# Kernel optimization log

Measured on AMD Instinct MI355X. Metric: run time of the kernel, lower is better.

Reference implementation:

```python
import jax, jax.numpy as jnp
import numpy as np

TEMPERATURE = 0.5
EPS = 1e-8  # torch cosine_similarity norm clamp


def setup_inputs() -> dict:
    key = jax.random.key(0)
    k1, k2, k3 = jax.random.split(key, 3)
    N, D = 4096, 256
    z_i = jax.random.normal(k1, (N, D), dtype=jnp.float32)
    z_j = jax.random.normal(k2, (N, D), dtype=jnp.float32)
    weights = jax.random.uniform(k3, (N,), dtype=jnp.float32)
    return {"z_i": z_i, "z_j": z_j, "weights": weights}


def reference(z_i, z_j, weights):
    N = z_i.shape[0]
    z = jnp.concatenate([z_i, z_j], axis=0)  # [2N, D]
    # cosine similarity via normalized matmul (same math as broadcasted F.cosine_similarity)
    norm = jnp.maximum(jnp.linalg.norm(z, axis=1, keepdims=True), EPS)
    zn = z / norm
    sim = zn @ zn.T  # [2N, 2N]
    # positives: diagonals at offsets +N and -N
    sim_ij = jnp.diagonal(sim, offset=N)
    sim_ji = jnp.diagonal(sim, offset=-N)
    positives = jnp.concatenate([sim_ij, sim_ji], axis=0)  # [2N]
    mask = 1.0 - jnp.eye(2 * N, dtype=sim.dtype)
    denominator = jnp.sum(mask * jnp.exp(sim / TEMPERATURE), axis=1)  # [2N]
    numerator = jnp.exp(positives / TEMPERATURE)
    all_losses = -jnp.log(numerator / denominator)  # [2N]
    w2 = jnp.tile(weights, 2)  # weights.repeat(2)
    loss = jnp.sum(all_losses * w2) / jnp.sum(w2)
    return loss
```

## Files before the change

### kernel.cpp

```cpp
#include <hip/hip_runtime.h>
#include <hip/hip_bf16.h>

#define PN   4096
#define PN2  8192
#define PD   256
#define TILE 128
#define NBLK (PN2 / TILE)
#define NTRI (NBLK * (NBLK + 1) / 2)

typedef __attribute__((ext_vector_type(8))) short bf16x8;
typedef __attribute__((ext_vector_type(4))) float f32x4;

typedef const __attribute__((address_space(1))) void* gas_ptr;
typedef __attribute__((address_space(3))) void* las_ptr;


__global__ __launch_bounds__(256) void normalize_kernel(
    const float* __restrict__ zi, const float* __restrict__ zj,
    __hip_bfloat16* __restrict__ zn, float* __restrict__ rowsum) {
  int r = blockIdx.x;
  int tid = threadIdx.x;
  const float* src = (r < PN) ? (zi + (size_t)r * PD) : (zj + (size_t)(r - PN) * PD);
  float x = src[tid];
  float s = x * x;
  #pragma unroll
  for (int off = 32; off >= 1; off >>= 1) s += __shfl_xor(s, off, 64);
  __shared__ float p[4];
  if ((tid & 63) == 0) p[tid >> 6] = s;
  __syncthreads();
  float tot = p[0] + p[1] + p[2] + p[3];
  float nrm = fmaxf(sqrtf(tot), 1e-8f);
  int g  = r >> 4, rr = r & 15;
  int c  = tid >> 5, q = (tid >> 3) & 3, j = tid & 7;
  zn[(size_t)(g * 8 + c) * 512 + q * 128 + rr * 8 + j] = __float2bfloat16(x / nrm);
  if (tid == 0) rowsum[r] = 0.0f;
}

__global__ __launch_bounds__(256, 2) void simsum_kernel(
    const __hip_bfloat16* __restrict__ zn,
    float* __restrict__ rowsum, float* __restrict__ pos) {
  __shared__ char As[64 * 1024];

  const int idx = blockIdx.x;
  int bj = (int)((sqrtf(8.0f * (float)idx + 1.0f) - 1.0f) * 0.5f);
  while ((bj + 1) * (bj + 2) / 2 <= idx) ++bj;
  while (bj * (bj + 1) / 2 > idx) --bj;
  const int bi = idx - bj * (bj + 1) / 2;
  const bool diagBlk = (bi == bj);
  const bool posBlk  = (bj == bi + PN / TILE);

  const int tid  = threadIdx.x;
  const int wave = tid >> 6;
  const int lane = tid & 63;
  const int quad = lane >> 4;
  const int c16  = lane & 15;
  const int wrow = bi * TILE + (wave >> 1) * 64;
  const int wcol = bj * TILE + (wave & 1) * 64;

  const char* aslab = (const char*)zn + (size_t)bi * 65536;
  #pragma unroll
  for (int p = 0; p < 16; ++p) {
    int off = (p * 4 + wave) * 1024;
    __builtin_amdgcn_global_load_lds((gas_ptr)(aslab + off + lane * 16),
                                     (las_ptr)(As + off), 16, 0, 0);
  }

  const __hip_bfloat16* bB[4];
  #pragma unroll
  for (int i = 0; i < 4; ++i)
    bB[i] = zn + (size_t)(bj * 8 + (wave & 1) * 4 + i) * 4096 + lane * 8;

  f32x4 acc[4][4];
  #pragma unroll
  for (int i = 0; i < 4; ++i)
    #pragma unroll
    for (int j = 0; j < 4; ++j)
      acc[i][j] = (f32x4){0.f, 0.f, 0.f, 0.f};

  const int arowg = (wave >> 1) * 4;

  __syncthreads();

  #pragma unroll
  for (int c = 0; c < 8; ++c) {
    bf16x8 a[4], b[4];
    #pragma unroll
    for (int ni = 0; ni < 4; ++ni) b[ni] = *(const bf16x8*)(bB[ni] + c * 512);
    #pragma unroll
    for (int mi = 0; mi < 4; ++mi)
      a[mi] = *(const bf16x8*)(As + ((arowg + mi) * 8 + c) * 1024 + lane * 16);
    #pragma unroll
    for (int mi = 0; mi < 4; ++mi)
      #pragma unroll
      for (int ni = 0; ni < 4; ++ni)
        acc[mi][ni] = __builtin_amdgcn_mfma_f32_16x16x32_bf16(a[mi], b[ni], acc[mi][ni], 0, 0, 0);
  }

  float colsum[4] = {0.f, 0.f, 0.f, 0.f};
  #pragma unroll
  for (int mi = 0; mi < 4; ++mi) {
    int rbase = wrow + mi * 16 + quad * 4;
    float rs[4] = {0.f, 0.f, 0.f, 0.f};
    #pragma unroll
    for (int ni = 0; ni < 4; ++ni) {
      int gcol = wcol + ni * 16 + c16;
      #pragma unroll
      for (int t = 0; t < 4; ++t) {
        int grow = rbase + t;
        float sim = acc[mi][ni][t];
        float e = __expf(2.0f * sim);
        if (diagBlk && gcol == grow) e = 0.0f;
        rs[t] += e;
        colsum[ni] += e;
        if (posBlk && gcol == grow + PN) {
          pos[grow] = sim;
          pos[grow + PN] = sim;
        }
      }
    }
    #pragma unroll
    for (int t = 0; t < 4; ++t) {
      #pragma unroll
      for (int off = 1; off <= 8; off <<= 1) rs[t] += __shfl_xor(rs[t], off, 64);
    }
    if (c16 == 0) {
      #pragma unroll
      for (int t = 0; t < 4; ++t) atomicAdd(&rowsum[rbase + t], rs[t]);
    }
  }
  if (!diagBlk) {
    #pragma unroll
    for (int ni = 0; ni < 4; ++ni) {
      float cs = colsum[ni];
      cs += __shfl_xor(cs, 16, 64);
      cs += __shfl_xor(cs, 32, 64);
      if (quad == 0) atomicAdd(&rowsum[wcol + ni * 16 + c16], cs);
    }
  }
}

__global__ __launch_bounds__(1024) void finalize_kernel(
    const float* __restrict__ rowsum, const float* __restrict__ pos,
    const float* __restrict__ w, float* __restrict__ out) {
  int tid = threadIdx.x;
  float wl = 0.f, ws = 0.f;
  for (int i = tid; i < PN2; i += 1024) {
    float li = logf(rowsum[i]) - 2.0f * pos[i];
    float wi = w[i & (PN - 1)];
    wl += wi * li;
    ws += wi;
  }
  #pragma unroll
  for (int off = 32; off >= 1; off >>= 1) {
    wl += __shfl_xor(wl, off, 64);
    ws += __shfl_xor(ws, off, 64);
  }
  __shared__ float pl[16], pw[16];
  if ((tid & 63) == 0) { pl[tid >> 6] = wl; pw[tid >> 6] = ws; }
  __syncthreads();
  if (tid == 0) {
    float sl = 0.f, sw = 0.f;
    #pragma unroll
    for (int k = 0; k < 16; ++k) { sl += pl[k]; sw += pw[k]; }
    out[0] = sl / sw;
  }
}

extern "C" void kernel_launch(void* const* d_in, const int* in_sizes, int n_in,
                              void* d_out, int out_size, void* d_ws, size_t ws_size,
                              hipStream_t stream) {
  const float* zi = (const float*)d_in[0];
  const float* zj = (const float*)d_in[1];
  const float* w  = (const float*)d_in[2];
  float* out = (float*)d_out;

  __hip_bfloat16* zn = (__hip_bfloat16*)d_ws;
  float* rowsum = (float*)((char*)d_ws + (size_t)PN2 * PD * 2);
  float* pos = rowsum + PN2;

  normalize_kernel<<<PN2, 256, 0, stream>>>(zi, zj, zn, rowsum);
  simsum_kernel<<<NTRI, 256, 0, stream>>>(zn, rowsum, pos);
  finalize_kernel<<<1, 1024, 0, stream>>>(rowsum, pos, w, out);
}
```

Baseline: 109.4 us.

## Fuse finalize into simsum via last-block ticket, vectorize normalize, prefetch B

Removes the separate finalize kernel launch: the last simsum block, chosen by an atomic ticket, does the weighted log reduction. The normalize kernel now handles one row per wave with float4 loads, and 4x fewer blocks. Simsum preloads half of the B fragments before the LDS barrier and prefetches the rest inside the loop. This raises register pressure and adds a threadfence plus an atomic per block.

```diff
diff --git a/kernel.cpp b/kernel.cpp
--- a/kernel.cpp
+++ b/kernel.cpp
@@ -17,29 +17,38 @@
 
 __global__ __launch_bounds__(256) void normalize_kernel(
     const float* __restrict__ zi, const float* __restrict__ zj,
-    __hip_bfloat16* __restrict__ zn, float* __restrict__ rowsum) {
-  int r = blockIdx.x;
-  int tid = threadIdx.x;
+    __hip_bfloat16* __restrict__ zn, float* __restrict__ rowsum,
+    unsigned int* __restrict__ ticket) {
+  const int tid  = threadIdx.x;
+  const int wave = tid >> 6;
+  const int lane = tid & 63;
+  const int r = blockIdx.x * 4 + wave;
   const float* src = (r < PN) ? (zi + (size_t)r * PD) : (zj + (size_t)(r - PN) * PD);
-  float x = src[tid];
-  float s = x * x;
+  f32x4 x = *(const f32x4*)(src + lane * 4);
+  float s = x.x * x.x + x.y * x.y + x.z * x.z + x.w * x.w;
   #pragma unroll
   for (int off = 32; off >= 1; off >>= 1) s += __shfl_xor(s, off, 64);
-  __shared__ float p[4];
-  if ((tid & 63) == 0) p[tid >> 6] = s;
-  __syncthreads();
-  float tot = p[0] + p[1] + p[2] + p[3];
-  float nrm = fmaxf(sqrtf(tot), 1e-8f);
-  int g  = r >> 4, rr = r & 15;
-  int c  = tid >> 5, q = (tid >> 3) & 3, j = tid & 7;
-  zn[(size_t)(g * 8 + c) * 512 + q * 128 + rr * 8 + j] = __float2bfloat16(x / nrm);
-  if (tid == 0) rowsum[r] = 0.0f;
+  float inv = 1.0f / fmaxf(sqrtf(s), 1e-8f);
+  int g = r >> 4, rr = r & 15;
+  __hip_bfloat16* dst = zn + (size_t)(g * 8 + (lane >> 3)) * 512
+                          + ((lane >> 1) & 3) * 128 + rr * 8 + (lane & 1) * 4;
+  __hip_bfloat16 tmp[4];
+  tmp[0] = __float2bfloat16(x.x * inv);
+  tmp[1] = __float2bfloat16(x.y * inv);
+  tmp[2] = __float2bfloat16(x.z * inv);
+  tmp[3] = __float2bfloat16(x.w * inv);
+  *(ushort4*)dst = *(ushort4*)tmp;
+  if (blockIdx.x < 32) rowsum[blockIdx.x * 256 + tid] = 0.0f;
+  if (blockIdx.x == 0 && tid == 0) *ticket = 0;
 }
 
 __global__ __launch_bounds__(256, 2) void simsum_kernel(
-    const __hip_bfloat16* __restrict__ zn,
-    float* __restrict__ rowsum, float* __restrict__ pos) {
+    const __hip_bfloat16* __restrict__ zn, float* __restrict__ rowsum,
+    float* __restrict__ pos, const float* __restrict__ w,
+    unsigned int* __restrict__ ticket, float* __restrict__ out) {
   __shared__ char As[64 * 1024];
+  __shared__ unsigned int tkt;
+  __shared__ float pl[4], pw[4];
 
   const int idx = blockIdx.x;
   int bj = (int)((sqrtf(8.0f * (float)idx + 1.0f) - 1.0f) * 0.5f);
@@ -70,6 +79,13 @@
   for (int i = 0; i < 4; ++i)
     bB[i] = zn + (size_t)(bj * 8 + (wave & 1) * 4 + i) * 4096 + lane * 8;
 
+  bf16x8 b[8][4];
+  #pragma unroll
+  for (int c = 0; c < 4; ++c)
+    #pragma unroll
+    for (int ni = 0; ni < 4; ++ni)
+      b[c][ni] = *(const bf16x8*)(bB[ni] + c * 512);
+
   f32x4 acc[4][4];
   #pragma unroll
   for (int i = 0; i < 4; ++i)
@@ -83,9 +99,12 @@
 
   #pragma unroll
   for (int c = 0; c < 8; ++c) {
-    bf16x8 a[4], b[4];
-    #pragma unroll
-    for (int ni = 0; ni < 4; ++ni) b[ni] = *(const bf16x8*)(bB[ni] + c * 512);
+    if (c < 4) {
+      #pragma unroll
+      for (int ni = 0; ni < 4; ++ni)
+        b[c + 4][ni] = *(const bf16x8*)(bB[ni] + (c + 4) * 512);
+    }
+    bf16x8 a[4];
     #pragma unroll
     for (int mi = 0; mi < 4; ++mi)
       a[mi] = *(const bf16x8*)(As + ((arowg + mi) * 8 + c) * 1024 + lane * 16);
@@ -93,7 +112,7 @@
     for (int mi = 0; mi < 4; ++mi)
       #pragma unroll
       for (int ni = 0; ni < 4; ++ni)
-        acc[mi][ni] = __builtin_amdgcn_mfma_f32_16x16x32_bf16(a[mi], b[ni], acc[mi][ni], 0, 0, 0);
+        acc[mi][ni] = __builtin_amdgcn_mfma_f32_16x16x32_bf16(a[mi], b[c][ni], acc[mi][ni], 0, 0, 0);
   }
 
   float colsum[4] = {0.f, 0.f, 0.f, 0.f};
@@ -113,8 +132,8 @@
         rs[t] += e;
         colsum[ni] += e;
         if (posBlk && gcol == grow + PN) {
-          pos[grow] = sim;
-          pos[grow + PN] = sim;
+          atomicExch(&pos[grow], sim);
+          atomicExch(&pos[grow + PN], sim);
         }
       }
     }
@@ -137,32 +156,30 @@
       if (quad == 0) atomicAdd(&rowsum[wcol + ni * 16 + c16], cs);
     }
   }
-}
-
-__global__ __launch_bounds__(1024) void finalize_kernel(
-    const float* __restrict__ rowsum, const float* __restrict__ pos,
-    const float* __restrict__ w, float* __restrict__ out) {
-  int tid = threadIdx.x;
-  float wl = 0.f, ws = 0.f;
-  for (int i = tid; i < PN2; i += 1024) {
-    float li = logf(rowsum[i]) - 2.0f * pos[i];
-    float wi = w[i & (PN - 1)];
-    wl += wi * li;
-    ws += wi;
-  }
-  #pragma unroll
-  for (int off = 32; off >= 1; off >>= 1) {
-    wl += __shfl_xor(wl, off, 64);
-    ws += __shfl_xor(ws, off, 64);
-  }
-  __shared__ float pl[16], pw[16];
-  if ((tid & 63) == 0) { pl[tid >> 6] = wl; pw[tid >> 6] = ws; }
+
+  __threadfence();
   __syncthreads();
-  if (tid == 0) {
-    float sl = 0.f, sw = 0.f;
-    #pragma unroll
-    for (int k = 0; k < 16; ++k) { sl += pl[k]; sw += pw[k]; }
-    out[0] = sl / sw;
+  if (tid == 0) tkt = atomicAdd(ticket, 1);
+  __syncthreads();
+  if (tkt == NTRI - 1) {
+    float wl = 0.f, wsum = 0.f;
+    for (int i = tid; i < PN2; i += 256) {
+      float rsv = __hip_atomic_load(&rowsum[i], __ATOMIC_RELAXED, __HIP_MEMORY_SCOPE_AGENT);
+      float pv  = __hip_atomic_load(&pos[i],    __ATOMIC_RELAXED, __HIP_MEMORY_SCOPE_AGENT);
+      float li = logf(rsv) - 2.0f * pv;
+      float wi = w[i & (PN - 1)];
+      wl += wi * li;
+      wsum += wi;
+    }
+    #pragma unroll
+    for (int off = 32; off >= 1; off >>= 1) {
+      wl += __shfl_xor(wl, off, 64);
+      wsum += __shfl_xor(wsum, off, 64);
+    }
+    if ((tid & 63) == 0) { pl[tid >> 6] = wl; pw[tid >> 6] = wsum; }
+    __syncthreads();
+    if (tid == 0)
+      out[0] = (pl[0] + pl[1] + pl[2] + pl[3]) / (pw[0] + pw[1] + pw[2] + pw[3]);
   }
 }
 
@@ -177,8 +194,8 @@
   __hip_bfloat16* zn = (__hip_bfloat16*)d_ws;
   float* rowsum = (float*)((char*)d_ws + (size_t)PN2 * PD * 2);
   float* pos = rowsum + PN2;
-
-  normalize_kernel<<<PN2, 256, 0, stream>>>(zi, zj, zn, rowsum);
-  simsum_kernel<<<NTRI, 256, 0, stream>>>(zn, rowsum, pos);
-  finalize_kernel<<<1, 1024, 0, stream>>>(rowsum, pos, w, out);
+  unsigned int* ticket = (unsigned int*)(pos + PN2);
+
+  normalize_kernel<<<PN2 / 4, 256, 0, stream>>>(zi, zj, zn, rowsum, ticket);
+  simsum_kernel<<<NTRI, 256, 0, stream>>>(zn, rowsum, pos, w, ticket, out);
 }
```

After: 219.8 us. +100.8%, slower.
